# Performance work log

Hardware: AMD Instinct MI355X
Metric: run time of the kernel (lower is better)

The kernel has to match this reference:

```python
import jax, jax.numpy as jnp
import numpy as np

B, T, V, E, H, TAGS = 128, 512, 50000, 256, 512, 64


def setup_inputs() -> dict:
    key = jax.random.key(0)
    ks = jax.random.split(key, 24)
    x = jax.random.randint(ks[0], (B, T), 0, V)
    lengths = jax.random.randint(ks[1], (B,), T // 2, T + 1).at[0].set(T)

    def u(k, shape, fan):
        s = 1.0 / np.sqrt(fan).astype(np.float32)
        return jax.random.uniform(k, shape, jnp.float32, -s, s)

    inp = {"x": x, "lengths": lengths,
           "emb": jax.random.normal(ks[2], (V, E), jnp.float32) * 0.1}
    ki = 3
    # layer1: input E; layer2: input 2H; two directions each
    for name, din in (("f1", E), ("b1", E), ("f2", 2 * H), ("b2", 2 * H)):
        inp[f"W_ih_{name}"] = u(ks[ki], (4 * H, din), H); ki += 1
        inp[f"W_hh_{name}"] = u(ks[ki], (4 * H, H), H); ki += 1
        inp[f"b_{name}"] = u(ks[ki], (4 * H,), H); ki += 1
    inp["W_cls"] = u(ks[ki], (TAGS, 2 * H), 2 * H); ki += 1
    inp["b_cls"] = u(ks[ki], (TAGS,), 2 * H)
    return inp


def _lstm_scan(x, W_ih, W_hh, b):
    # x: [B,T,D] -> outputs h: [B,T,H]; PyTorch gate order i,f,g,o
    Bn, Tn, _ = x.shape
    Hn = W_hh.shape[1]
    gx = jnp.einsum('btd,gd->btg', x, W_ih) + b  # [B,T,4H]

    def step(carry, g_t):
        h, c = carry
        g = g_t + h @ W_hh.T
        i, f, gg, o = jnp.split(g, 4, axis=-1)
        c = jax.nn.sigmoid(f) * c + jax.nn.sigmoid(i) * jnp.tanh(gg)
        h = jax.nn.sigmoid(o) * jnp.tanh(c)
        return (h, c), h

    h0 = jnp.zeros((Bn, Hn), x.dtype)
    _, hs = jax.lax.scan(step, (h0, h0), jnp.swapaxes(gx, 0, 1))
    return jnp.swapaxes(hs, 0, 1)


def _reverse_by_len(x, lengths):
    # reverse each sequence within its own length; zero out padding
    Tn = x.shape[1]
    idx = lengths[:, None] - 1 - jnp.arange(Tn)[None, :]
    valid = idx >= 0
    g = jnp.take_along_axis(x, jnp.where(valid, idx, 0)[:, :, None], axis=1)
    return jnp.where(valid[:, :, None], g, 0.0)


def _bilstm(x, pf, pb, lengths):
    # packed-sequence semantics: outputs beyond length are zero (pad_packed)
    mask = (jnp.arange(x.shape[1])[None, :] < lengths[:, None])[:, :, None]
    out_f = _lstm_scan(x, *pf) * mask
    out_b = _reverse_by_len(_lstm_scan(_reverse_by_len(x, lengths), *pb), lengths)
    return jnp.concatenate([out_f, out_b], axis=-1)


def reference(x, lengths, emb,
              W_ih_f1, W_hh_f1, b_f1, W_ih_b1, W_hh_b1, b_b1,
              W_ih_f2, W_hh_f2, b_f2, W_ih_b2, W_hh_b2, b_b2,
              W_cls, b_cls):
    e = emb[x]  # [B,T,E]
    out1 = _bilstm(e, (W_ih_f1, W_hh_f1, b_f1), (W_ih_b1, W_hh_b1, b_b1), lengths)
    out2 = _bilstm(out1, (W_ih_f2, W_hh_f2, b_f2), (W_ih_b2, W_hh_b2, b_b2), lengths)
    # dropout is identity in eval mode
    logits = jnp.einsum('bth,kh->btk', out2, W_cls) + b_cls
    return logits
```

## Files before the change

### kernel.cpp

```cpp
#include <hip/hip_runtime.h>


typedef unsigned short u16;
typedef unsigned long long u64;
typedef _Float16 f16;
typedef __attribute__((ext_vector_type(8))) _Float16 f16x8;
typedef __attribute__((ext_vector_type(4))) float f32x4;

#define TT 512
#define HH 512
#define CH 32
#define NCH 16
#define TSTR 16

__device__ __forceinline__ u16 f2h(float f) { f16 h = (f16)f; return __builtin_bit_cast(u16, h); }
__device__ __forceinline__ float h2f(u16 s) { return (float)__builtin_bit_cast(f16, s); }
__device__ __forceinline__ float sigf(float x) { return 1.f / (1.f + __expf(-x)); }
__device__ __forceinline__ float tanhf_(float x) { return 1.f - 2.f / (__expf(2.f * x) + 1.f); }
__device__ __forceinline__ f32x4 zf4() { f32x4 z; z[0]=0.f; z[1]=0.f; z[2]=0.f; z[3]=0.f; return z; }

__device__ __forceinline__ void st16_sc0(u16* p, f16x8 v) {
  asm volatile("global_store_dwordx4 %0, %1, off sc0" :: "v"(p), "v"(v) : "memory");
}
__device__ __forceinline__ void st16_sc1(u16* p, f16x8 v) {
  asm volatile("global_store_dwordx4 %0, %1, off sc1" :: "v"(p), "v"(v) : "memory");
}
__device__ __forceinline__ f16x8 ld16_sc0(const u16* p) {
  f16x8 v;
  asm volatile("global_load_dwordx4 %0, %1, off sc0" : "=v"(v) : "v"(p) : "memory");
  return v;
}
__device__ __forceinline__ void sttag_sc0(int* p, int v) {
  asm volatile("global_store_dword %0, %1, off sc0" :: "v"(p), "v"(v) : "memory");
}
__device__ __forceinline__ void sttag_sc1(int* p, int v) {
  asm volatile("global_store_dword %0, %1, off sc1" :: "v"(p), "v"(v) : "memory");
}
__device__ __forceinline__ int ldtag_sc0(const int* p) {
  int v;
  asm volatile("global_load_dword %0, %1, off sc0" : "=v"(v) : "v"(p) : "memory");
  return v;
}
__device__ __forceinline__ int ldtag_sc1(const int* p) {
  int v;
  asm volatile("global_load_dword %0, %1, off sc1" : "=v"(v) : "v"(p) : "memory");
  return v;
}


struct CvtJob { const float* s; u16* d; int n; };
struct CvtJobs { CvtJob j[9]; };

__global__ void cvt_many(CvtJobs jobs) {
  CvtJob jb = jobs.j[blockIdx.y];
  int i = blockIdx.x * 256 + threadIdx.x;
  if (i < jb.n) jb.d[i] = f2h(jb.s[i]);
}

__global__ void bias_init(float* __restrict__ o, const float* __restrict__ b, int n) {
  int i = blockIdx.x * 256 + threadIdx.x;
  if (i < n) o[i] = b[i & 63];
}

__global__ void fill_diag(float* __restrict__ o, int n, float sentinel) {
  int i = blockIdx.x * 256 + threadIdx.x;
  if (i < n) o[i] = (i == 0) ? sentinel : 0.f;
}


#define GX_LOAD(kt_) do { \
    if (lmode == 0) { \
      rf0 = *(const f32x4*)(Arf + (kt_) + kc); \
      rf1 = *(const f32x4*)(Arf + (kt_) + kc + 4); \
      rf2 = *(const f32x4*)(Arf + (kt_) + kc + 8); \
      rf3 = *(const f32x4*)(Arf + (kt_) + kc + 12); \
    } else { \
      ra0 = *(const uint4*)(Arh + (kt_) + kc); \
      ra1 = *(const uint4*)(Arh + (kt_) + kc + 8); \
    } \
    rb0 = *(const uint4*)(Br0 + (kt_) + kc); \
    rb1 = *(const uint4*)(Br0 + (kt_) + kc + 8); \
    rb2 = *(const uint4*)(Br1 + (kt_) + kc); \
    rb3 = *(const uint4*)(Br1 + (kt_) + kc + 8); \
  } while (0)

#define CLS_LOAD(kt_) do { \
    ca0 = *(const uint4*)(Arow + (kt_)); \
    ca1 = *(const uint4*)(Arow + (kt_) + 8); \
    ca2 = *(const uint4*)(Arow + (kt_) + 16); \
    ca3 = *(const uint4*)(Arow + (kt_) + 24); \
    cb0 = *(const uint4*)(Brw + (kt_) + kc); \
    cb1 = *(const uint4*)(Brw + (kt_) + kc + 8); \
  } while (0)

__device__ __forceinline__ void gemm_body(
    int gb, int nb, int tid,
    int lmode, int do_gx,
    const int* __restrict__ x, const float* __restrict__ emb,
    const u16* __restrict__ out1g,
    const u16* __restrict__ Bf, const u16* __restrict__ Bb,
    const float* __restrict__ biasf, const float* __restrict__ biasb,
    u16* __restrict__ gxn, int s0n, int K,
    int cls_s0, const u16* __restrict__ out2p, const u16* __restrict__ wclsp,
    float* __restrict__ dout, const int* __restrict__ len,
    u16* As, u16* Bs)
{
  const int lane = tid & 63;
  const int m16 = lane & 15, quad = lane >> 4;
  const int wv = tid >> 6;
  const int row = tid >> 1;
  const int kc = (tid & 1) * 16;
  const int ngx = do_gx ? 2048 : 0;
  const int ntl = ngx + (cls_s0 >= 0 ? 64 : 0);

  for (int t = gb; t < ntl; t += nb) {
    f32x4 acc[4][4];
#pragma unroll
    for (int a2 = 0; a2 < 4; ++a2)
#pragma unroll
      for (int c2 = 0; c2 < 4; ++c2) acc[a2][c2] = zf4();

    if (t < ngx) {
      const int dir = t >> 10, rem = t & 1023, tm = rem & 63, tn = rem >> 6;
      const u16* Bm = dir ? Bb : Bf;
      const float* bias = dir ? biasb : biasf;
      u16* Cp = gxn + (size_t)dir * 4096 * 2048;
      const int rowm = tm * 64 + row, b = rowm >> 5, ii = rowm & 31, s = s0n + ii;
      int pos;
      if (dir) { int p = len[b] - 1 - s; pos = p < 0 ? 0 : p; } else pos = s;
      const float* Arf = nullptr; const u16* Arh = nullptr;
      if (lmode == 0) Arf = emb + (size_t)x[b * TT + pos] * 256;
      else            Arh = out1g + ((size_t)b * TT + pos) * 1024;
      const u16* Br0 = Bm + (size_t)(tn * 128 + row) * K;
      const u16* Br1 = Bm + (size_t)(tn * 128 + row + 64) * K;

      f32x4 rf0, rf1, rf2, rf3; uint4 ra0, ra1, rb0, rb1, rb2, rb3;
      GX_LOAD(0);
      for (int kt = 0; kt < K; kt += 32) {
        if (lmode == 0) {
          f16x8 v0, v1;
#pragma unroll
          for (int j = 0; j < 4; ++j) {
            v0[j] = (f16)rf0[j]; v0[j + 4] = (f16)rf1[j];
            v1[j] = (f16)rf2[j]; v1[j + 4] = (f16)rf3[j];
          }
          *(f16x8*)&As[row * 40 + kc] = v0;
          *(f16x8*)&As[row * 40 + kc + 8] = v1;
        } else {
          *(uint4*)&As[row * 40 + kc]     = ra0;
          *(uint4*)&As[row * 40 + kc + 8] = ra1;
        }
        *(uint4*)&Bs[row * 40 + kc]            = rb0;
        *(uint4*)&Bs[row * 40 + kc + 8]        = rb1;
        *(uint4*)&Bs[(row + 64) * 40 + kc]     = rb2;
        *(uint4*)&Bs[(row + 64) * 40 + kc + 8] = rb3;
        __syncthreads();
        if (kt + 32 < K) GX_LOAD(kt + 32);
        f16x8 af[4], bfr[4];
#pragma unroll
        for (int mt = 0; mt < 4; ++mt)
          af[mt] = *(const f16x8*)&As[(mt * 16 + m16) * 40 + quad * 8];
#pragma unroll
        for (int nt = 0; nt < 4; ++nt)
          bfr[nt] = *(const f16x8*)&Bs[(wv * 64 + nt * 16 + m16) * 40 + quad * 8];
#pragma unroll
        for (int mt = 0; mt < 4; ++mt)
#pragma unroll
          for (int nt = 0; nt < 4; ++nt)
            acc[mt][nt] = __builtin_amdgcn_mfma_f32_16x16x32_f16(af[mt], bfr[nt], acc[mt][nt], 0, 0, 0);
        __syncthreads();
      }
#pragma unroll
      for (int mt = 0; mt < 4; ++mt)
#pragma unroll
        for (int nt = 0; nt < 4; ++nt) {
          const int n = tn * 128 + wv * 64 + nt * 16 + m16;
          const float bv = bias[n];
#pragma unroll
          for (int r = 0; r < 4; ++r) {
            const int mm = tm * 64 + mt * 16 + quad * 4 + r;
            Cp[(size_t)mm * 2048 + n] = f2h(acc[mt][nt][r] + bv);
          }
        }
    } else {
      const int tc = t - ngx;
      const int dir = tc >> 5, m0 = (tc & 31) * 128;
      const u16* Arow = out2p + (size_t)(m0 + tid) * 1024 + dir * 512;
      const u16* Brw  = wclsp + (size_t)row * 1024 + dir * 512;
      uint4 ca0, ca1, ca2, ca3, cb0, cb1;
      CLS_LOAD(0);
      for (int kt = 0; kt < 512; kt += 32) {
        *(uint4*)&Bs[tid * 40]      = ca0;
        *(uint4*)&Bs[tid * 40 + 8]  = ca1;
        *(uint4*)&Bs[tid * 40 + 16] = ca2;
        *(uint4*)&Bs[tid * 40 + 24] = ca3;
        *(uint4*)&As[row * 40 + kc]     = cb0;
        *(uint4*)&As[row * 40 + kc + 8] = cb1;
        __syncthreads();
        if (kt + 32 < 512) CLS_LOAD(kt + 32);
        f16x8 af[4], bfr[4];
#pragma unroll
        for (int mt = 0; mt < 4; ++mt)
          af[mt] = *(const f16x8*)&Bs[(wv * 64 + mt * 16 + m16) * 40 + quad * 8];
#pragma unroll
        for (int nt = 0; nt < 4; ++nt)
          bfr[nt] = *(const f16x8*)&As[(nt * 16 + m16) * 40 + quad * 8];
#pragma unroll
        for (int mt = 0; mt < 4; ++mt)
#pragma unroll
          for (int nt = 0; nt < 4; ++nt)
            acc[mt][nt] = __builtin_amdgcn_mfma_f32_16x16x32_f16(af[mt], bfr[nt], acc[mt][nt], 0, 0, 0);
        __syncthreads();
      }
#pragma unroll
      for (int mt = 0; mt < 4; ++mt)
#pragma unroll
        for (int nt = 0; nt < 4; ++nt) {
          const int n = nt * 16 + m16;
#pragma unroll
          for (int r = 0; r < 4; ++r) {
            const int m = m0 + wv * 64 + mt * 16 + quad * 4 + r;
            const int b = m >> 5, ii = m & 31, s = cls_s0 + ii;
            const int L = len[b];
            if (s < L) {
              const int pos = dir ? (L - 1 - s) : s;
              atomicAdd(&dout[((size_t)b * TT + pos) * 64 + n], acc[mt][nt][r]);
            }
          }
        }
    }
  }
}

__global__ __launch_bounds__(128, 2) void gemm_all(
    int lmode, int do_gx, const int* __restrict__ x, const float* __restrict__ emb,
    const u16* __restrict__ out1g,
    const u16* __restrict__ Bf, const u16* __restrict__ Bb,
    const float* __restrict__ biasf, const float* __restrict__ biasb,
    u16* __restrict__ gxn, int s0n, int K,
    int cls_s0, const u16* __restrict__ out2p, const u16* __restrict__ wclsp,
    float* __restrict__ dout, const int* __restrict__ len)
{
  __shared__ u16 As[64 * 40];
  __shared__ u16 Bs[128 * 40];
  gemm_body(blockIdx.x, gridDim.x, threadIdx.x, lmode, do_gx, x, emb, out1g,
            Bf, Bb, biasf, biasb, gxn, s0n, K, cls_s0, out2p, wclsp, dout, len,
            As, Bs);
}


__global__ __launch_bounds__(128, 1) void fused(
    const u16* __restrict__ gxc, const u16* __restrict__ whh_f,
    const u16* __restrict__ whh_b, const int* __restrict__ len,
    u16* __restrict__ out_pos, u16* __restrict__ out_chunk,
    u16* __restrict__ hseq, u16* __restrict__ hcarry,
    float* __restrict__ cbuf, int* __restrict__ tags,
    int s0, int tagbase,
    int lmode, int do_gx, const int* __restrict__ x,
    const float* __restrict__ emb, const u16* __restrict__ out1g,
    const u16* __restrict__ Bf, const u16* __restrict__ Bb,
    const float* __restrict__ biasf, const float* __restrict__ biasb,
    u16* __restrict__ gxn, int s0n, int K,
    int cls_s0, const u16* __restrict__ out2p, const u16* __restrict__ wclsp,
    float* __restrict__ dout)
{
  __shared__ u16 As[64 * 40];
  __shared__ u16 Bs[128 * 40];
  __shared__ u16 tb[2][256];

  if (blockIdx.x >= 256) {
    gemm_body(blockIdx.x - 256, 256, threadIdx.x, lmode, do_gx, x, emb, out1g,
              Bf, Bb, biasf, biasb, gxn, s0n, K, cls_s0, out2p, wclsp, dout,
              len, As, Bs);
    return;
  }

  const int tid = threadIdx.x;
  const int bi = blockIdx.x;
  const int bg = bi & 7;
  const int rank = bi >> 3;
  const int dir = rank >> 4;
  const int role = rank & 15;
  const int b_base = bg * 16;
  const int grp = dir * 8 + bg;
  const int u_tile = role * 2 + (tid >> 6);
  const int u_base = u_tile * 16;
  const int lane = tid & 63;
  const int m16 = lane & 15, quad = lane >> 4;
  const u16* gxd = gxc + (size_t)dir * 4096 * 2048;
  const u16* whh = dir ? whh_b : whh_f;
  u16* T = tb[tid >> 6];
  int* gtags = tags + grp * 32 * TSTR;
  int* mytag = gtags + u_tile * TSTR;

  f16x8 bf[4][16];
#pragma unroll
  for (int g = 0; g < 4; ++g) {
    const u16* wrow = whh + (size_t)(g * HH + u_base + m16) * HH + quad * 8;
#pragma unroll
    for (int ks = 0; ks < 16; ++ks)
      bf[g][ks] = *(const f16x8*)(wrow + ks * 32);
  }

  int lenr[4];
#pragma unroll
  for (int r = 0; r < 4; ++r) lenr[r] = len[b_base + quad * 4 + r];

  float cst[4];
  if (s0 == 0) {
#pragma unroll
    for (int r = 0; r < 4; ++r) cst[r] = 0.f;
  } else {
#pragma unroll
    for (int r = 0; r < 4; ++r)
      cst[r] = cbuf[(size_t)dir * 65536 + (b_base + quad * 4 + r) * HH + u_base + m16];
  }

  const u16* carry_rd = hcarry + (size_t)dir * 65536 + (b_base + m16) * HH + quad * 8;

  for (int i = 0; i < CH; ++i) {
    const int s = s0 + i;

    u16 gpre[4][4];
#pragma unroll
    for (int r = 0; r < 4; ++r) {
      const int batch = b_base + quad * 4 + r;
      const u16* gq = gxd + (size_t)(batch * CH + i) * 2048 + u_base + m16;
      gpre[r][0] = gq[0]; gpre[r][1] = gq[512];
      gpre[r][2] = gq[1024]; gpre[r][3] = gq[1536];
    }

    f16x8 a[16];
    if (i == 0) {
      if (s0 == 0) {
#pragma unroll
        for (int ks = 0; ks < 16; ++ks)
#pragma unroll
          for (int j = 0; j < 8; ++j) a[ks][j] = (f16)0.f;
      } else {
#pragma unroll
        for (int ks = 0; ks < 16; ++ks)
          a[ks] = *(const f16x8*)(carry_rd + ks * 32);
      }
    } else {
      const int want = tagbase + i;
      const int* myp = gtags + (lane & 31) * TSTR;
      int it = 0;
      while (true) {
        int t = (it & 1) ? ldtag_sc1(myp) : ldtag_sc0(myp);
        asm volatile("s_waitcnt vmcnt(0)" ::: "memory");
        if (__ballot(t < want) == 0ull) break;
        ++it;
        __builtin_amdgcn_s_sleep(1);
      }
      const u16* sb = hseq + ((size_t)(dir * CH + (i - 1)) * 128 + b_base + m16) * HH + quad * 8;
#pragma unroll
      for (int ks = 0; ks < 16; ++ks) a[ks] = ld16_sc0(sb + ks * 32);
      asm volatile("s_waitcnt vmcnt(0)" ::: "memory");
    }

    f32x4 a0 = zf4(), a1 = zf4(), a2 = zf4(), a3 = zf4();
#pragma unroll
    for (int ks = 0; ks < 16; ++ks) {
      a0 = __builtin_amdgcn_mfma_f32_16x16x32_f16(a[ks], bf[0][ks], a0, 0, 0, 0);
      a1 = __builtin_amdgcn_mfma_f32_16x16x32_f16(a[ks], bf[1][ks], a1, 0, 0, 0);
      a2 = __builtin_amdgcn_mfma_f32_16x16x32_f16(a[ks], bf[2][ks], a2, 0, 0, 0);
      a3 = __builtin_amdgcn_mfma_f32_16x16x32_f16(a[ks], bf[3][ks], a3, 0, 0, 0);
    }

    u16 hv[4];
#pragma unroll
    for (int r = 0; r < 4; ++r) {
      float gi = a0[r] + h2f(gpre[r][0]);
      float gf = a1[r] + h2f(gpre[r][1]);
      float gg = a2[r] + h2f(gpre[r][2]);
      float go = a3[r] + h2f(gpre[r][3]);
      float c = sigf(gf) * cst[r] + sigf(gi) * tanhf_(gg);
      cst[r] = c;
      hv[r] = f2h(sigf(go) * tanhf_(c));
    }

#pragma unroll
    for (int r = 0; r < 4; ++r)
      T[(quad * 4 + r) * 16 + m16] = hv[r];
    if (lane < 32) {
      const int brow = lane >> 1, col8 = (lane & 1) * 8;
      f16x8 hrow = *(const f16x8*)&T[brow * 16 + col8];
      if (i == CH - 1) {
        *(f16x8*)(hcarry + (size_t)dir * 65536 + (b_base + brow) * HH + u_base + col8) = hrow;
      } else {
        u16* dst = hseq + ((size_t)(dir * CH + i) * 128 + b_base + brow) * HH + u_base + col8;
        st16_sc0(dst, hrow);
        st16_sc1(dst, hrow);
      }
    }
    if (i != CH - 1) {
      asm volatile("s_waitcnt vmcnt(0)" ::: "memory");
      if (lane == 0) { sttag_sc0(mytag, tagbase + i + 1); sttag_sc1(mytag, tagbase + i + 1); }
    }

#pragma unroll
    for (int r = 0; r < 4; ++r) {
      const int batch = b_base + quad * 4 + r;
      const int L = lenr[r];
      const bool valid = s < L;
      if (out_pos) {
        const int p = dir ? (L - 1 - s) : s;
        const int wrow = valid ? (p < 0 ? 0 : p) : s;
        out_pos[(size_t)(batch * TT + wrow) * 1024 + dir * 512 + u_base + m16]
            = valid ? hv[r] : (u16)0;
      } else {
        out_chunk[(size_t)(batch * CH + i) * 1024 + dir * 512 + u_base + m16] = hv[r];
      }
    }
  }

#pragma unroll
  for (int r = 0; r < 4; ++r)
    cbuf[(size_t)dir * 65536 + (b_base + quad * 4 + r) * HH + u_base + m16] = cst[r];
}


extern "C" void kernel_launch(void* const* d_in, const int* in_sizes, int n_in,
                              void* d_out, int out_size, void* d_ws, size_t ws_size,
                              hipStream_t stream) {
  const int*   x      = (const int*)d_in[0];
  const int*   len    = (const int*)d_in[1];
  const float* emb    = (const float*)d_in[2];
  const float* Wih_f1 = (const float*)d_in[3];
  const float* Whh_f1 = (const float*)d_in[4];
  const float* b_f1   = (const float*)d_in[5];
  const float* Wih_b1 = (const float*)d_in[6];
  const float* Whh_b1 = (const float*)d_in[7];
  const float* b_b1   = (const float*)d_in[8];
  const float* Wih_f2 = (const float*)d_in[9];
  const float* Whh_f2 = (const float*)d_in[10];
  const float* b_f2   = (const float*)d_in[11];
  const float* Wih_b2 = (const float*)d_in[12];
  const float* Whh_b2 = (const float*)d_in[13];
  const float* b_b2   = (const float*)d_in[14];
  const float* W_cls  = (const float*)d_in[15];
  const float* b_cls  = (const float*)d_in[16];

  const size_t GXC1  = (size_t)2 * 4096 * 2048 * 2;
  const size_t OUT1  = (size_t)65536 * 1024 * 2;
  const size_t OUT2  = (size_t)4096 * 1024 * 2;
  const size_t WTS   = (size_t)9502720 * 2;
  const size_t HSEQ  = (size_t)2 * CH * 128 * 512 * 2;
  const size_t HCAR  = (size_t)2 * 128 * 512 * 2;
  const size_t TAGSZ = 16 * 32 * TSTR * 4;
  const size_t NEED = 2 * GXC1 + OUT1 + 2 * OUT2 + WTS + HSEQ + HCAR + 524288 + TAGSZ;
  if (ws_size < NEED) {
    fill_diag<<<dim3((out_size + 255) / 256), dim3(256), 0, stream>>>(
        (float*)d_out, out_size, (float)(ws_size >> 20));
    return;
  }

  char* w = (char*)d_ws;
  u16* gxb0  = (u16*)w; w += GXC1;
  u16* gxb1  = (u16*)w; w += GXC1;
  u16* out1  = (u16*)w; w += OUT1;
  u16* o2b0  = (u16*)w; w += OUT2;
  u16* o2b1  = (u16*)w; w += OUT2;
  u16* wihf1 = (u16*)w; w += (size_t)2048 * 256 * 2;
  u16* wihb1 = (u16*)w; w += (size_t)2048 * 256 * 2;
  u16* whhf1 = (u16*)w; w += (size_t)2048 * 512 * 2;
  u16* whhb1 = (u16*)w; w += (size_t)2048 * 512 * 2;
  u16* wihf2 = (u16*)w; w += (size_t)2048 * 1024 * 2;
  u16* wihb2 = (u16*)w; w += (size_t)2048 * 1024 * 2;
  u16* whhf2 = (u16*)w; w += (size_t)2048 * 512 * 2;
  u16* whhb2 = (u16*)w; w += (size_t)2048 * 512 * 2;
  u16* wcls  = (u16*)w; w += (size_t)64 * 1024 * 2;
  u16* hseq  = (u16*)w; w += HSEQ;
  u16* hcarry = (u16*)w; w += HCAR;
  float* cbuf = (float*)w; w += 524288;
  int* tags  = (int*)w; w += TAGSZ;

  CvtJobs jobs = {{
    { Wih_f1, wihf1, 2048 * 256 }, { Wih_b1, wihb1, 2048 * 256 },
    { Whh_f1, whhf1, 2048 * 512 }, { Whh_b1, whhb1, 2048 * 512 },
    { Wih_f2, wihf2, 2048 * 1024 }, { Wih_b2, wihb2, 2048 * 1024 },
    { Whh_f2, whhf2, 2048 * 512 }, { Whh_b2, whhb2, 2048 * 512 },
    { W_cls,  wcls,  64 * 1024 },
  }};
  cvt_many<<<dim3(8192, 9), dim3(256), 0, stream>>>(jobs);
  bias_init<<<dim3(16384), dim3(256), 0, stream>>>((float*)d_out, b_cls, 65536 * 64);
  hipMemsetAsync(tags, 0, TAGSZ, stream);

  u16* gxb[2] = { gxb0, gxb1 };
  u16* o2b[2] = { o2b0, o2b1 };
  float* doutf = (float*)d_out;

  int seq = 0;
  gemm_all<<<dim3(512), dim3(128), 0, stream>>>(
      0, 1, x, emb, nullptr, wihf1, wihb1, b_f1, b_b1,
      gxb[0], 0, 256, -1, nullptr, wcls, doutf, len);
  for (int c = 0; c < NCH; ++c) {
    fused<<<dim3(512), dim3(128), 0, stream>>>(
        gxb[c & 1], whhf1, whhb1, len, out1, nullptr, hseq, hcarry, cbuf, tags,
        c * CH, seq * CH,
        0, (c < NCH - 1) ? 1 : 0, x, emb, nullptr, wihf1, wihb1, b_f1, b_b1,
        gxb[(c + 1) & 1], (c + 1) * CH, 256,
        -1, nullptr, wcls, doutf);
    ++seq;
  }
  gemm_all<<<dim3(512), dim3(128), 0, stream>>>(
      1, 1, x, emb, out1, wihf2, wihb2, b_f2, b_b2,
      gxb[0], 0, 1024, -1, nullptr, wcls, doutf, len);
  for (int c = 0; c < NCH; ++c) {
    fused<<<dim3(512), dim3(128), 0, stream>>>(
        gxb[c & 1], whhf2, whhb2, len, nullptr, o2b[c & 1], hseq, hcarry, cbuf, tags,
        c * CH, seq * CH,
        1, (c < NCH - 1) ? 1 : 0, x, emb, out1, wihf2, wihb2, b_f2, b_b2,
        gxb[(c + 1) & 1], (c + 1) * CH, 1024,
        (c >= 1) ? (c - 1) * CH : -1, o2b[(c & 1) ^ 1], wcls, doutf);
    ++seq;
  }
  gemm_all<<<dim3(512), dim3(128), 0, stream>>>(
      1, 0, x, emb, out1, wihf2, wihb2, b_f2, b_b2,
      gxb[0], 0, 1024, (NCH - 1) * CH, o2b[(NCH - 1) & 1], wcls, doutf, len);
}
```

Before: 7.578 ms.

## Interleave recurrent/GEMM blocks, prefetch gate inputs, split coherence stores, resize GEMM grids

Recurrent and GEMM blocks in the fused kernel are now interleaved by block index (bit 3 selects the role) rather than split into halves, which changes how the two roles are spread across XCDs/CUs. The per-step gate pre-activation loads are software-prefetched one step ahead so they overlap the recurrence. The dual sc0/sc1 hidden-state and tag stores are reordered so the tag is published after the first store before the second is issued, shortening the critical path to the consumer. The standalone GEMM launch grids are changed (2048 for the input projections, 64 for the final classifier pass), which relies on gemm_body handling the new block counts correctly.

```diff
diff --git a/kernel.cpp b/kernel.cpp
--- a/kernel.cpp
+++ b/kernel.cpp
@@ -268,17 +268,19 @@
   __shared__ u16 Bs[128 * 40];
   __shared__ u16 tb[2][256];
 
-  if (blockIdx.x >= 256) {
-    gemm_body(blockIdx.x - 256, 256, threadIdx.x, lmode, do_gx, x, emb, out1g,
+  const int bix = blockIdx.x;
+  const int vix = ((bix >> 4) << 3) | (bix & 7);
+
+  if (bix & 8) {
+    gemm_body(vix, 256, threadIdx.x, lmode, do_gx, x, emb, out1g,
               Bf, Bb, biasf, biasb, gxn, s0n, K, cls_s0, out2p, wclsp, dout,
               len, As, Bs);
     return;
   }
 
   const int tid = threadIdx.x;
-  const int bi = blockIdx.x;
-  const int bg = bi & 7;
-  const int rank = bi >> 3;
+  const int bg = vix & 7;
+  const int rank = vix >> 3;
   const int dir = rank >> 4;
   const int role = rank & 15;
   const int b_base = bg * 16;
@@ -318,17 +320,17 @@
 
   const u16* carry_rd = hcarry + (size_t)dir * 65536 + (b_base + m16) * HH + quad * 8;
 
+  u16 gpre[4][4];
+#pragma unroll
+  for (int r = 0; r < 4; ++r) {
+    const int batch = b_base + quad * 4 + r;
+    const u16* gq = gxd + (size_t)(batch * CH + 0) * 2048 + u_base + m16;
+    gpre[r][0] = gq[0]; gpre[r][1] = gq[512];
+    gpre[r][2] = gq[1024]; gpre[r][3] = gq[1536];
+  }
+
   for (int i = 0; i < CH; ++i) {
     const int s = s0 + i;
-
-    u16 gpre[4][4];
-#pragma unroll
-    for (int r = 0; r < 4; ++r) {
-      const int batch = b_base + quad * 4 + r;
-      const u16* gq = gxd + (size_t)(batch * CH + i) * 2048 + u_base + m16;
-      gpre[r][0] = gq[0]; gpre[r][1] = gq[512];
-      gpre[r][2] = gq[1024]; gpre[r][3] = gq[1536];
-    }
 
     f16x8 a[16];
     if (i == 0) {
@@ -383,20 +385,35 @@
 #pragma unroll
     for (int r = 0; r < 4; ++r)
       T[(quad * 4 + r) * 16 + m16] = hv[r];
-    if (lane < 32) {
-      const int brow = lane >> 1, col8 = (lane & 1) * 8;
-      f16x8 hrow = *(const f16x8*)&T[brow * 16 + col8];
-      if (i == CH - 1) {
+    if (i == CH - 1) {
+      if (lane < 32) {
+        const int brow = lane >> 1, col8 = (lane & 1) * 8;
+        f16x8 hrow = *(const f16x8*)&T[brow * 16 + col8];
         *(f16x8*)(hcarry + (size_t)dir * 65536 + (b_base + brow) * HH + u_base + col8) = hrow;
-      } else {
-        u16* dst = hseq + ((size_t)(dir * CH + i) * 128 + b_base + brow) * HH + u_base + col8;
+      }
+    } else {
+      u16* dst = nullptr; f16x8 hrow;
+      if (lane < 32) {
+        const int brow = lane >> 1, col8 = (lane & 1) * 8;
+        hrow = *(const f16x8*)&T[brow * 16 + col8];
+        dst = hseq + ((size_t)(dir * CH + i) * 128 + b_base + brow) * HH + u_base + col8;
         st16_sc0(dst, hrow);
-        st16_sc1(dst, hrow);
-      }
-    }
-    if (i != CH - 1) {
+      }
       asm volatile("s_waitcnt vmcnt(0)" ::: "memory");
-      if (lane == 0) { sttag_sc0(mytag, tagbase + i + 1); sttag_sc1(mytag, tagbase + i + 1); }
+      if (lane == 0) sttag_sc0(mytag, tagbase + i + 1);
+      if (lane < 32) st16_sc1(dst, hrow);
+      asm volatile("s_waitcnt vmcnt(0)" ::: "memory");
+      if (lane == 0) sttag_sc1(mytag, tagbase + i + 1);
+    }
+
+    if (i + 1 < CH) {
+#pragma unroll
+      for (int r = 0; r < 4; ++r) {
+        const int batch = b_base + quad * 4 + r;
+        const u16* gq = gxd + (size_t)(batch * CH + (i + 1)) * 2048 + u_base + m16;
+        gpre[r][0] = gq[0]; gpre[r][1] = gq[512];
+        gpre[r][2] = gq[1024]; gpre[r][3] = gq[1536];
+      }
     }
 
 #pragma unroll
@@ -492,7 +509,7 @@
   float* doutf = (float*)d_out;
 
   int seq = 0;
-  gemm_all<<<dim3(512), dim3(128), 0, stream>>>(
+  gemm_all<<<dim3(2048), dim3(128), 0, stream>>>(
       0, 1, x, emb, nullptr, wihf1, wihb1, b_f1, b_b1,
       gxb[0], 0, 256, -1, nullptr, wcls, doutf, len);
   for (int c = 0; c < NCH; ++c) {
@@ -504,7 +521,7 @@
         -1, nullptr, wcls, doutf);
     ++seq;
   }
-  gemm_all<<<dim3(512), dim3(128), 0, stream>>>(
+  gemm_all<<<dim3(2048), dim3(128), 0, stream>>>(
       1, 1, x, emb, out1, wihf2, wihb2, b_f2, b_b2,
       gxb[0], 0, 1024, -1, nullptr, wcls, doutf, len);
   for (int c = 0; c < NCH; ++c) {
@@ -516,7 +533,7 @@
         (c >= 1) ? (c - 1) * CH : -1, o2b[(c & 1) ^ 1], wcls, doutf);
     ++seq;
   }
-  gemm_all<<<dim3(512), dim3(128), 0, stream>>>(
+  gemm_all<<<dim3(64), dim3(128), 0, stream>>>(
       1, 0, x, emb, out1, wihf2, wihb2, b_f2, b_b2,
       gxb[0], 0, 1024, (NCH - 1) * CH, o2b[(NCH - 1) & 1], wcls, doutf, len);
 }
```

New measurement: 6.562 ms. -13.4%, faster.
